# Optimization experiments

Hardware: AMD Instinct MI355X
Metric: run time of the kernel (lower is better)

## Reference

```python
import jax, jax.numpy as jnp
import numpy as np

SIGMA = 10.0   # collision energy prefactor (init kwarg sigma)
LCOL = 0.5     # collision length scale (init kwarg lcol)
N_CHAINS = 2
CONF_LEN = 16388  # 4 header entries + 2 * 8192 step angles


def _chain_energy(conf):
    # conf: (CONF_LEN,) ; entries 0..3 only feed a zeroed init position
    c = conf[4:] + 0.5                     # (2N,) in [0,1]
    r1, r2 = c[0::2], c[1::2]              # (N,), (N,)
    ph = r1 * (2.0 * jnp.pi)
    th = jnp.arccos(1.0 - 2.0 * r2)
    sth = jnp.sin(th)
    steps = jnp.stack([sth * jnp.cos(ph), sth * jnp.sin(ph), jnp.cos(th)], axis=1)  # (N,3) unit vectors
    steps = jnp.concatenate([jnp.zeros((1, 3), conf.dtype), steps], axis=0)        # prepend origin
    pos = jnp.cumsum(steps, axis=0)        # (M,3) polymer positions, M = N+1
    # squared pairwise distances via Gram trick: ||a-b||^2 = |a|^2 + |b|^2 - 2 a.b
    sq = jnp.sum(pos * pos, axis=1)        # (M,)
    d2 = sq[:, None] + sq[None, :] - 2.0 * (pos @ pos.T)  # (M,M)
    d2 = jnp.maximum(d2, 0.0)              # clamp fp negatives
    # torch: sigma * sum(exp(-(cdist/lcol)^2)) == sigma * sum(exp(-d2/lcol^2))
    return SIGMA * jnp.sum(jnp.exp(-d2 / (LCOL * LCOL)))


def setup_inputs() -> dict:
    key = jax.random.key(0)
    confdata = jax.random.uniform(key, (N_CHAINS, CONF_LEN), dtype=jnp.float32,
                                  minval=-0.5, maxval=0.5)
    return {"confdata": confdata}


def reference(confdata):
    # sum of per-chain energies (torch loops over chains and accumulates)
    return jnp.sum(jax.vmap(_chain_energy)(confdata))
```

## Files before the change

### kernel.cpp

```cpp
#include <hip/hip_runtime.h>
#include <math.h>

#define N_CHAINS 2
#define CONF_LEN 16388
#define NSTEPS   8192
#define NPOS     8193
#define TILE     256
#define NTILES   33
#define NPAD     (NTILES * TILE)
#define NPAIRT   (NTILES * (NTILES + 1) / 2)
#define SIGMA    10.0f
#define ALPHA    3.3972887f
#define D2CUT    460.0f
#define PTHREADS 1024
#define NPAIRS   4096
#define ROWS     (NPAIRS / PTHREADS)

__device__ float4 g_pos[N_CHAINS * NPAD];
__device__ float4 g_aabb_min[N_CHAINS * NTILES];
__device__ float4 g_aabb_max[N_CHAINS * NTILES];

__device__ __forceinline__ float exp2_fast(float x) {
#if __has_builtin(__builtin_amdgcn_exp2f)
    return __builtin_amdgcn_exp2f(x);
#else
    return exp2f(x);
#endif
}

__global__ __launch_bounds__(1024) void pos_kernel(const float* __restrict__ conf,
                                                   float* __restrict__ out) {
    const int chain = blockIdx.x;
    const int t = threadIdx.x;
    const int lane = t & 63;
    const int w = t >> 6;
    const float TWO_PI = 6.2831853071795864769f;

    const float4* cin = (const float4*)(conf + chain * CONF_LEN + 4);
    float4* cpos = g_pos + chain * NPAD;

    __shared__ float lds[48];

    if (chain == 0 && t == 0) out[0] = 0.0f;
    if (t == 0) cpos[0] = make_float4(0.f, 0.f, 0.f, 0.f);

    float Rx = 0.f, Ry = 0.f, Rz = 0.f;

    for (int m = 0; m < ROWS; ++m) {
        const int p = t + PTHREADS * m;
        float4 q = cin[p];

        float sp0, cp0, sp1, cp1;
        __sincosf((q.x + 0.5f) * TWO_PI, &sp0, &cp0);
        float ct0 = 1.0f - 2.0f * (q.y + 0.5f);
        float st0 = sqrtf(fmaxf(0.f, 1.0f - ct0 * ct0));
        __sincosf((q.z + 0.5f) * TWO_PI, &sp1, &cp1);
        float ct1 = 1.0f - 2.0f * (q.w + 0.5f);
        float st1 = sqrtf(fmaxf(0.f, 1.0f - ct1 * ct1));
        float ux0 = st0 * cp0, uy0 = st0 * sp0, uz0 = ct0;
        float ux1 = st1 * cp1, uy1 = st1 * sp1, uz1 = ct1;
        float sx = ux0 + ux1, sy = uy0 + uy1, sz = uz0 + uz1;

        float ix = sx, iy = sy, iz = sz;
        for (int off = 1; off < 64; off <<= 1) {
            float nx = __shfl_up(ix, off, 64);
            float ny = __shfl_up(iy, off, 64);
            float nz = __shfl_up(iz, off, 64);
            if (lane >= off) { ix += nx; iy += ny; iz += nz; }
        }
        float ex = __shfl_up(ix, 1, 64);
        float ey = __shfl_up(iy, 1, 64);
        float ez = __shfl_up(iz, 1, 64);
        if (lane == 0) { ex = 0.f; ey = 0.f; ez = 0.f; }
        __syncthreads();
        if (lane == 63) { lds[w] = ix; lds[16 + w] = iy; lds[32 + w] = iz; }
        __syncthreads();
        float wox = 0.f, woy = 0.f, woz = 0.f;
        float tox = 0.f, toy = 0.f, toz = 0.f;
        for (int w2 = 0; w2 < 16; ++w2) {
            float ax = lds[w2], ay = lds[16 + w2], az = lds[32 + w2];
            tox += ax; toy += ay; toz += az;
            if (w2 < w) { wox += ax; woy += ay; woz += az; }
        }

        float bx = Rx + wox + ex, by = Ry + woy + ey, bz = Rz + woz + ez;
        float x1 = bx + ux0, y1 = by + uy0, z1 = bz + uz0;
        float x2 = bx + sx,  y2 = by + sy,  z2 = bz + sz;
        float X1 = x1 * ALPHA, Y1 = y1 * ALPHA, Z1 = z1 * ALPHA;
        float X2 = x2 * ALPHA, Y2 = y2 * ALPHA, Z2 = z2 * ALPHA;
        float B1 = -0.5f * (X1 * X1 + Y1 * Y1 + Z1 * Z1);
        float B2 = -0.5f * (X2 * X2 + Y2 * Y2 + Z2 * Z2);
        cpos[2 * p + 1] = make_float4(X1, Y1, Z1, B1);
        cpos[2 * p + 2] = make_float4(X2, Y2, Z2, B2);

        Rx += tox; Ry += toy; Rz += toz;
    }

    for (int idx = NPOS + t; idx < NPAD; idx += PTHREADS) {
        cpos[idx] = make_float4(0.f, 0.f, 0.f, -1.0e30f);
    }
    __syncthreads();

    for (int rep = 0; rep < 3; ++rep) {
        if (rep == 2 && w != 0) break;
        const int tau = (rep == 0) ? w : (rep == 1 ? w + 16 : 32);
        float mnx = 1e30f, mny = 1e30f, mnz = 1e30f;
        float mxx = -1e30f, mxy = -1e30f, mxz = -1e30f;
        for (int j = 0; j < 4; ++j) {
            float4 pt = cpos[tau * TILE + lane + 64 * j];
            mnx = fminf(mnx, pt.x); mny = fminf(mny, pt.y); mnz = fminf(mnz, pt.z);
            mxx = fmaxf(mxx, pt.x); mxy = fmaxf(mxy, pt.y); mxz = fmaxf(mxz, pt.z);
        }
        for (int off = 32; off > 0; off >>= 1) {
            mnx = fminf(mnx, __shfl_down(mnx, off, 64));
            mny = fminf(mny, __shfl_down(mny, off, 64));
            mnz = fminf(mnz, __shfl_down(mnz, off, 64));
            mxx = fmaxf(mxx, __shfl_down(mxx, off, 64));
            mxy = fmaxf(mxy, __shfl_down(mxy, off, 64));
            mxz = fmaxf(mxz, __shfl_down(mxz, off, 64));
        }
        if (lane == 0) {
            g_aabb_min[chain * NTILES + tau] = make_float4(mnx, mny, mnz, 0.f);
            g_aabb_max[chain * NTILES + tau] = make_float4(mxx, mxy, mxz, 0.f);
        }
    }
}

__global__ __launch_bounds__(256) void pair_kernel(float* __restrict__ out) {
    int b = blockIdx.x;
    const int chain = b / NPAIRT;
    int p = b % NPAIRT;
    int ti = 0;
    while (true) {
        int rl = NTILES - ti;
        if (p < rl) break;
        p -= rl;
        ++ti;
    }
    const int tj = ti + p;

    float4 mni = g_aabb_min[chain * NTILES + ti];
    float4 mxi = g_aabb_max[chain * NTILES + ti];
    float4 mnj = g_aabb_min[chain * NTILES + tj];
    float4 mxj = g_aabb_max[chain * NTILES + tj];
    float dx = fmaxf(0.f, fmaxf(mni.x - mxj.x, mnj.x - mxi.x));
    float dy = fmaxf(0.f, fmaxf(mni.y - mxj.y, mnj.y - mxi.y));
    float dz = fmaxf(0.f, fmaxf(mni.z - mxj.z, mnj.z - mxi.z));
    if (fmaf(dx, dx, fmaf(dy, dy, dz * dz)) > D2CUT) return;

    const int t = threadIdx.x;
    const float4* cpos = g_pos + chain * NPAD;

    __shared__ float4 sj[TILE];
    sj[t] = cpos[tj * TILE + t];
    __syncthreads();

    const float4 pi4 = cpos[ti * TILE + t];
    const float xi = pi4.x, yi = pi4.y, zi = pi4.z, Ai = pi4.w;

    float acc = 0.f;
#pragma unroll 8
    for (int j = 0; j < TILE; ++j) {
        float4 q = sj[j];
        float E = fmaf(xi, q.x, fmaf(yi, q.y, fmaf(zi, q.z, Ai + q.w)));
        acc += exp2_fast(E);
    }

    acc *= (ti == tj) ? SIGMA : 2.0f * SIGMA;

    for (int off = 32; off > 0; off >>= 1) acc += __shfl_down(acc, off, 64);
    __shared__ float wsum[4];
    if ((t & 63) == 0) wsum[t >> 6] = acc;
    __syncthreads();
    if (t == 0) atomicAdd(out, wsum[0] + wsum[1] + wsum[2] + wsum[3]);
}

extern "C" void kernel_launch(void* const* d_in, const int* in_sizes, int n_in,
                              void* d_out, int out_size, void* d_ws, size_t ws_size,
                              hipStream_t stream) {
    const float* conf = (const float*)d_in[0];
    float* out = (float*)d_out;

    pos_kernel<<<N_CHAINS, PTHREADS, 0, stream>>>(conf, out);
    pair_kernel<<<N_CHAINS * NPAIRT, TILE, 0, stream>>>(out);
}
```

Before: 82.49 us.

## Tighten tile-pair cutoff, pad with last position, use revolution-based sin/cos

The squared-distance cutoff for skipping tile pairs drops from 460 to 64 in scaled units, so more far-apart tile pairs are culled and fewer exp2 evaluations run. Padding entries now copy the last chain position instead of the origin, which keeps the final tile's bounding box tight. The position kernel uses hardware sin/cos that take revolutions, and replaces the serial per-wave offset loop with a 16-lane shuffle scan. The tighter cutoff drops more small energy terms, each below roughly 2^-32, so results are approximated slightly more than before.

```diff
diff --git a/kernel.cpp b/kernel.cpp
--- a/kernel.cpp
+++ b/kernel.cpp
@@ -11,7 +11,7 @@
 #define NPAIRT   (NTILES * (NTILES + 1) / 2)
 #define SIGMA    10.0f
 #define ALPHA    3.3972887f
-#define D2CUT    460.0f
+#define D2CUT    64.0f
 #define PTHREADS 1024
 #define NPAIRS   4096
 #define ROWS     (NPAIRS / PTHREADS)
@@ -27,6 +27,20 @@
     return exp2f(x);
 #endif
 }
+__device__ __forceinline__ float sin_rev(float x) {
+#if __has_builtin(__builtin_amdgcn_sinf)
+    return __builtin_amdgcn_sinf(x);
+#else
+    return __sinf(x * 6.2831853071795864769f);
+#endif
+}
+__device__ __forceinline__ float cos_rev(float x) {
+#if __has_builtin(__builtin_amdgcn_cosf)
+    return __builtin_amdgcn_cosf(x);
+#else
+    return __cosf(x * 6.2831853071795864769f);
+#endif
+}
 
 __global__ __launch_bounds__(1024) void pos_kernel(const float* __restrict__ conf,
                                                    float* __restrict__ out) {
@@ -34,12 +48,12 @@
     const int t = threadIdx.x;
     const int lane = t & 63;
     const int w = t >> 6;
-    const float TWO_PI = 6.2831853071795864769f;
 
     const float4* cin = (const float4*)(conf + chain * CONF_LEN + 4);
     float4* cpos = g_pos + chain * NPAD;
 
-    __shared__ float lds[48];
+    __shared__ float lwx[16], lwy[16], lwz[16];
+    __shared__ float lox[17], loy[17], loz[17];
 
     if (chain == 0 && t == 0) out[0] = 0.0f;
     if (t == 0) cpos[0] = make_float4(0.f, 0.f, 0.f, 0.f);
@@ -50,13 +64,12 @@
         const int p = t + PTHREADS * m;
         float4 q = cin[p];
 
-        float sp0, cp0, sp1, cp1;
-        __sincosf((q.x + 0.5f) * TWO_PI, &sp0, &cp0);
-        float ct0 = 1.0f - 2.0f * (q.y + 0.5f);
-        float st0 = sqrtf(fmaxf(0.f, 1.0f - ct0 * ct0));
-        __sincosf((q.z + 0.5f) * TWO_PI, &sp1, &cp1);
-        float ct1 = 1.0f - 2.0f * (q.w + 0.5f);
-        float st1 = sqrtf(fmaxf(0.f, 1.0f - ct1 * ct1));
+        float sp0 = sin_rev(q.x + 0.5f), cp0 = cos_rev(q.x + 0.5f);
+        float ct0 = -2.0f * q.y;
+        float st0 = sqrtf(fmaxf(0.f, fmaf(-ct0, ct0, 1.0f)));
+        float sp1 = sin_rev(q.z + 0.5f), cp1 = cos_rev(q.z + 0.5f);
+        float ct1 = -2.0f * q.w;
+        float st1 = sqrtf(fmaxf(0.f, fmaf(-ct1, ct1, 1.0f)));
         float ux0 = st0 * cp0, uy0 = st0 * sp0, uz0 = ct0;
         float ux1 = st1 * cp1, uy1 = st1 * sp1, uz1 = ct1;
         float sx = ux0 + ux1, sy = uy0 + uy1, sz = uz0 + uz1;
@@ -68,22 +81,26 @@
             float nz = __shfl_up(iz, off, 64);
             if (lane >= off) { ix += nx; iy += ny; iz += nz; }
         }
-        float ex = __shfl_up(ix, 1, 64);
-        float ey = __shfl_up(iy, 1, 64);
-        float ez = __shfl_up(iz, 1, 64);
-        if (lane == 0) { ex = 0.f; ey = 0.f; ez = 0.f; }
+        float ex = ix - sx, ey = iy - sy, ez = iz - sz;
+
         __syncthreads();
-        if (lane == 63) { lds[w] = ix; lds[16 + w] = iy; lds[32 + w] = iz; }
+        if (lane == 63) { lwx[w] = ix; lwy[w] = iy; lwz[w] = iz; }
         __syncthreads();
-        float wox = 0.f, woy = 0.f, woz = 0.f;
-        float tox = 0.f, toy = 0.f, toz = 0.f;
-        for (int w2 = 0; w2 < 16; ++w2) {
-            float ax = lds[w2], ay = lds[16 + w2], az = lds[32 + w2];
-            tox += ax; toy += ay; toz += az;
-            if (w2 < w) { wox += ax; woy += ay; woz += az; }
-        }
-
-        float bx = Rx + wox + ex, by = Ry + woy + ey, bz = Rz + woz + ez;
+        if (t < 16) {
+            float vx = lwx[t], vy = lwy[t], vz = lwz[t];
+            float jx = vx, jy = vy, jz = vz;
+            for (int off = 1; off < 16; off <<= 1) {
+                float nx = __shfl_up(jx, off, 64);
+                float ny = __shfl_up(jy, off, 64);
+                float nz = __shfl_up(jz, off, 64);
+                if (t >= off) { jx += nx; jy += ny; jz += nz; }
+            }
+            lox[t] = jx - vx; loy[t] = jy - vy; loz[t] = jz - vz;
+            if (t == 15) { lox[16] = jx; loy[16] = jy; loz[16] = jz; }
+        }
+        __syncthreads();
+
+        float bx = Rx + lox[w] + ex, by = Ry + loy[w] + ey, bz = Rz + loz[w] + ez;
         float x1 = bx + ux0, y1 = by + uy0, z1 = bz + uz0;
         float x2 = bx + sx,  y2 = by + sy,  z2 = bz + sz;
         float X1 = x1 * ALPHA, Y1 = y1 * ALPHA, Z1 = z1 * ALPHA;
@@ -93,11 +110,13 @@
         cpos[2 * p + 1] = make_float4(X1, Y1, Z1, B1);
         cpos[2 * p + 2] = make_float4(X2, Y2, Z2, B2);
 
-        Rx += tox; Ry += toy; Rz += toz;
-    }
-
+        Rx += lox[16]; Ry += loy[16]; Rz += loz[16];
+    }
+    __syncthreads();
+
+    float4 last = cpos[NPOS - 1];
     for (int idx = NPOS + t; idx < NPAD; idx += PTHREADS) {
-        cpos[idx] = make_float4(0.f, 0.f, 0.f, -1.0e30f);
+        cpos[idx] = make_float4(last.x, last.y, last.z, -1.0e30f);
     }
     __syncthreads();
 
```

Result: no change. 81.37 us, median of 2 (-1.4%).
